# Performance work log

Hardware: AMD Instinct MI355X
Metric: run time of the kernel (lower is better)

Reference implementation:

```python
import jax, jax.numpy as jnp
import numpy as np

B, DIM, HEADS, AGENT = 16, 256, 8, 49
POOL = 7  # int(sqrt(agent_num))


def _pool_matrix(size, out):
    # PyTorch AdaptiveAvgPool2d bin boundaries: start=floor(i*size/out), end=ceil((i+1)*size/out)
    P = np.zeros((out, size), np.float32)
    for i in range(out):
        s = (i * size) // out
        e = -((-(i + 1) * size) // out)
        P[i, s:e] = 1.0 / (e - s)
    return jnp.asarray(P)


def _forward(x, Wq, Wkv, Wproj, bproj, Wdwc, bdwc,
             an_bias, na_bias, ah_bias, aw_bias, ha_bias, wa_bias, H, W):
    b, c, h, w = x.shape
    n = H * W
    head_dim = c // HEADS
    scale = head_dim ** -0.5
    xt = x.reshape(b, c, n).transpose(0, 2, 1)            # [b, n, c]
    q = xt @ Wq.T                                          # [b, n, c]
    kv = xt @ Wkv.T
    k, v = jnp.split(kv, 2, axis=-1)
    # agent tokens: adaptive avg pool of q over the HxW grid -> 7x7
    qimg = q.reshape(b, H, W, c)
    Ph, Pw = _pool_matrix(H, POOL), _pool_matrix(W, POOL)
    agent = jnp.einsum('ph,qw,bhwc->bpqc', Ph, Pw, qimg).reshape(b, AGENT, c)

    def to_heads(t):
        return t.reshape(b, -1, HEADS, head_dim).transpose(0, 2, 1, 3)

    qh, kh, vh, ah = to_heads(q), to_heads(k), to_heads(v), to_heads(agent)

    # stage 1: agent -> kv attention with interpolated position bias
    pb1 = jax.image.resize(an_bias, (HEADS, AGENT, H, W), method='bilinear').reshape(HEADS, AGENT, n)
    pb2 = (ah_bias + aw_bias).reshape(1, HEADS, AGENT, n)
    pos_bias = pb1[None] + pb2                             # [1/b, h, 49, n]
    agent_attn = jax.nn.softmax(jnp.einsum('bhad,bhnd->bhan', ah * scale, kh) + pos_bias, axis=-1)
    agent_v = jnp.einsum('bhan,bhnd->bhad', agent_attn, vh)  # [b, h, 49, d]

    # stage 2: query -> agent attention
    ab1 = jax.image.resize(na_bias, (HEADS, AGENT, H, W), method='bilinear').reshape(HEADS, AGENT, n).transpose(0, 2, 1)
    ab2 = (ha_bias + wa_bias).reshape(1, HEADS, n, AGENT)
    agent_bias = ab1[None] + ab2                           # [1/b, h, n, 49]
    q_attn = jax.nn.softmax(jnp.einsum('bhnd,bhad->bhna', qh * scale, ah) + agent_bias, axis=-1)
    out = jnp.einsum('bhna,bhad->bhnd', q_attn, agent_v).transpose(0, 2, 1, 3).reshape(b, n, c)

    # depthwise conv residual on v
    vimg = vh.transpose(0, 2, 1, 3).reshape(b, H, W, c).transpose(0, 3, 1, 2)  # [b, c, H, W]
    dw = jax.lax.conv_general_dilated(vimg, Wdwc, (1, 1), 'SAME',
                                      feature_group_count=c,
                                      dimension_numbers=('NCHW', 'OIHW', 'NCHW'))
    dw = dw + bdwc[None, :, None, None]
    out = out + dw.transpose(0, 2, 3, 1).reshape(b, n, c)
    out = out @ Wproj.T + bproj
    return out.transpose(0, 2, 1).reshape(b, c, h, w)


def setup_inputs() -> dict:
    key = jax.random.key(0)
    ks = jax.random.split(key, 12)
    s = 0.02
    return {
        'x': jax.random.normal(ks[0], (B, DIM, 64, 64), jnp.float32),
        'Wq': jax.random.normal(ks[1], (DIM, DIM), jnp.float32) * s,
        'Wkv': jax.random.normal(ks[2], (2 * DIM, DIM), jnp.float32) * s,
        'Wproj': jax.random.normal(ks[3], (DIM, DIM), jnp.float32) * s,
        'bproj': jnp.zeros((DIM,), jnp.float32),
        'Wdwc': jax.random.normal(ks[4], (DIM, 1, 3, 3), jnp.float32) * s,
        'bdwc': jnp.zeros((DIM,), jnp.float32),
        'an_bias': jax.random.normal(ks[5], (HEADS, AGENT, 7, 7), jnp.float32) * s,
        'na_bias': jax.random.normal(ks[6], (HEADS, AGENT, 7, 7), jnp.float32) * s,
        'ah_bias': jax.random.normal(ks[7], (1, HEADS, AGENT, 64, 1), jnp.float32) * s,
        'aw_bias': jax.random.normal(ks[8], (1, HEADS, AGENT, 1, 64), jnp.float32) * s,
        'ha_bias': jax.random.normal(ks[9], (1, HEADS, 64, 1, AGENT), jnp.float32) * s,
        'wa_bias': jax.random.normal(ks[10], (1, HEADS, 1, 64, AGENT), jnp.float32) * s,
        'H': 64,
        'W': 64,
    }


def reference(x, Wq, Wkv, Wproj, bproj, Wdwc, bdwc,
              an_bias, na_bias, ah_bias, aw_bias, ha_bias, wa_bias, H, W):
    return _forward(x, Wq, Wkv, Wproj, bproj, Wdwc, bdwc,
                    an_bias, na_bias, ah_bias, aw_bias, ha_bias, wa_bias, H, W)
```

## Files before the change

kernel.cpp:

```cpp
#include <hip/hip_runtime.h>
#include <hip/hip_bf16.h>
#include <stdint.h>

using bf16 = __hip_bfloat16;

#define SCALE 0.17677669529663687f

typedef short short8 __attribute__((ext_vector_type(8)));
typedef float f32x4 __attribute__((ext_vector_type(4)));

__device__ __forceinline__ float bf2f(bf16 v) { return __bfloat162float(v); }

__device__ __forceinline__ unsigned short f2bf(float f) {
    unsigned int u = __float_as_uint(f);
    unsigned int r = u + 0x7fffu + ((u >> 16) & 1u);
    return (unsigned short)(r >> 16);
}

__device__ __forceinline__ void load8bf(const bf16* p, float* f) {
    uint4 u = *reinterpret_cast<const uint4*>(p);
    f[0] = __uint_as_float(u.x << 16); f[1] = __uint_as_float(u.x & 0xffff0000u);
    f[2] = __uint_as_float(u.y << 16); f[3] = __uint_as_float(u.y & 0xffff0000u);
    f[4] = __uint_as_float(u.z << 16); f[5] = __uint_as_float(u.z & 0xffff0000u);
    f[6] = __uint_as_float(u.w << 16); f[7] = __uint_as_float(u.w & 0xffff0000u);
}

__device__ __forceinline__ void gload16(const void* g, void* l) {
    __builtin_amdgcn_global_load_lds(
        (const __attribute__((address_space(1))) void*)g,
        (__attribute__((address_space(3))) void*)l, 16, 0, 0);
}

__global__ __launch_bounds__(256) void convert_w(
    const float* __restrict__ Wq, const float* __restrict__ Wkv,
    const float* __restrict__ Wp,
    bf16* __restrict__ Wqkv_bf, bf16* __restrict__ Wp_bf)
{
    int row = blockIdx.x, tid = threadIdx.x;
    const float* src; bf16* dst;
    if (row < 768) {
        src = (row < 256) ? Wq + (size_t)row * 256 : Wkv + (size_t)(row - 256) * 256;
        dst = Wqkv_bf + (size_t)row * 256;
    } else {
        src = Wp + (size_t)(row - 768) * 256;
        dst = Wp_bf + (size_t)(row - 768) * 256;
    }
    *reinterpret_cast<unsigned short*>(dst + tid) = f2bf(src[tid]);
}

__global__ __launch_bounds__(256) void qkv_mfma(
    const float* __restrict__ x, const bf16* __restrict__ Wqkv,
    bf16* __restrict__ q, bf16* __restrict__ k, bf16* __restrict__ v)
{
    __shared__ __align__(16) short As[128 * 36];
    __shared__ __align__(16) short Bs[128 * 32];
    const int j0 = blockIdx.x * 128;
    const int b  = blockIdx.y >> 5;
    const int m0 = (blockIdx.y & 31) * 128;
    const int tid = threadIdx.x;
    const int w = tid >> 6, lane = tid & 63;
    const int wm = w & 1, wn = w >> 1;
    const int quad = lane >> 4, ln = lane & 15;

    const float* Ax = x + (size_t)(b * 256) * 4096 + m0;
    const short* Bg = (const short*)Wqkv + (size_t)j0 * 256;
    const int ldrow = lane >> 2;
    const int ldcol = (lane & 3) * 8;
    const int c4 = (tid >> 5) * 4;
    const int p4 = (tid & 31) * 4;

    f32x4 acc[4][4] = {};

    for (int k0 = 0; k0 < 256; k0 += 32) {
        __syncthreads();
        #pragma unroll
        for (int p = 0; p < 2; ++p) {
            int row = w * 32 + p * 16;
            gload16(Bg + (size_t)(row + ldrow) * 256 + k0 + ldcol, Bs + row * 32);
        }
        float4 xr[4];
        #pragma unroll
        for (int j = 0; j < 4; ++j)
            xr[j] = *reinterpret_cast<const float4*>(
                Ax + (size_t)(k0 + c4 + j) * 4096 + p4);
        #pragma unroll
        for (int pp = 0; pp < 4; ++pp) {
            unsigned short t4[4];
            t4[0] = f2bf(((const float*)&xr[0])[pp]);
            t4[1] = f2bf(((const float*)&xr[1])[pp]);
            t4[2] = f2bf(((const float*)&xr[2])[pp]);
            t4[3] = f2bf(((const float*)&xr[3])[pp]);
            *reinterpret_cast<uint2*>(&As[(p4 + pp) * 36 + c4]) =
                *reinterpret_cast<const uint2*>(t4);
        }
        __syncthreads();
        short8 af[4], bfr[4];
        #pragma unroll
        for (int mi = 0; mi < 4; ++mi)
            af[mi] = *reinterpret_cast<const short8*>(&As[(wm * 64 + mi * 16 + ln) * 36 + quad * 8]);
        #pragma unroll
        for (int ni = 0; ni < 4; ++ni)
            bfr[ni] = *reinterpret_cast<const short8*>(&Bs[(wn * 64 + ni * 16 + ln) * 32 + quad * 8]);
        #pragma unroll
        for (int mi = 0; mi < 4; ++mi)
            #pragma unroll
            for (int ni = 0; ni < 4; ++ni)
                acc[mi][ni] = __builtin_amdgcn_mfma_f32_16x16x32_bf16(
                    af[mi], bfr[ni], acc[mi][ni], 0, 0, 0);
    }

    bf16* dst; int cb;
    if (j0 < 256)      { dst = q; cb = j0; }
    else if (j0 < 512) { dst = k; cb = j0 - 256; }
    else               { dst = v; cb = j0 - 512; }
    #pragma unroll
    for (int mi = 0; mi < 4; ++mi)
        #pragma unroll
        for (int r = 0; r < 4; ++r) {
            int pos = m0 + wm * 64 + mi * 16 + quad * 4 + r;
            unsigned short* o = reinterpret_cast<unsigned short*>(
                dst + ((size_t)(b * 4096 + pos)) * 256 + cb + wn * 64 + ln);
            #pragma unroll
            for (int ni = 0; ni < 4; ++ni)
                o[ni * 16] = f2bf(acc[mi][ni][r]);
        }
}

__global__ __launch_bounds__(256) void pool_agent(
    const bf16* __restrict__ q, float* __restrict__ agent)
{
    int bid = blockIdx.x;
    int b = bid / 49, a = bid % 49;
    int py = a / 7, px = a % 7;
    int ys = (py * 64) / 7, ye = ((py + 1) * 64 + 6) / 7;
    int xs = (px * 64) / 7, xe = ((px + 1) * 64 + 6) / 7;
    int ch = threadIdx.x;
    float s = 0.f;
    for (int y = ys; y < ye; ++y)
        for (int x = xs; x < xe; ++x)
            s += bf2f(q[((size_t)(b * 4096) + y * 64 + x) * 256 + ch]);
    agent[((size_t)(b * 49) + a) * 256 + ch] = s / (float)((ye - ys) * (xe - xs));
}

__global__ __launch_bounds__(256) void make_pbias(
    const float* __restrict__ an, const float* __restrict__ ahb,
    const float* __restrict__ awb, float* __restrict__ pbias)
{
    int bid = blockIdx.x;
    __shared__ float bb[49], ay[64], ax[64];
    int tid = threadIdx.x;
    if (tid < 49) bb[tid] = an[(size_t)bid * 49 + tid];
    if (tid < 64) {
        ay[tid] = ahb[(size_t)bid * 64 + tid];
        ax[tid] = awb[(size_t)bid * 64 + tid];
    }
    __syncthreads();
    for (int it = 0; it < 16; ++it) {
        int pos = it * 256 + tid;
        int y = pos >> 6, x = pos & 63;
        float fy = (y + 0.5f) * (7.f / 64.f) - 0.5f; fy = fminf(fmaxf(fy, 0.f), 6.f);
        float fx = (x + 0.5f) * (7.f / 64.f) - 0.5f; fx = fminf(fmaxf(fx, 0.f), 6.f);
        int y0 = (int)fy, x0 = (int)fx;
        int y1 = min(y0 + 1, 6), x1 = min(x0 + 1, 6);
        float wy = fy - y0, wx = fx - x0;
        float val = (1.f - wy) * ((1.f - wx) * bb[y0 * 7 + x0] + wx * bb[y0 * 7 + x1])
                  + wy * ((1.f - wx) * bb[y1 * 7 + x0] + wx * bb[y1 * 7 + x1]);
        pbias[(size_t)bid * 4096 + pos] = val + ay[y] + ax[x];
    }
}

__global__ __launch_bounds__(256) void make_abias2(
    const float* __restrict__ na, const float* __restrict__ hab,
    const float* __restrict__ wab, bf16* __restrict__ ab2)
{
    const int h = blockIdx.x, p0 = blockIdx.y * 256;
    const int tid = threadIdx.x;
    __shared__ float bb[49 * 49];
    __shared__ float hy[64 * 49];
    __shared__ float wxs[64 * 49];
    for (int i = tid; i < 49 * 49; i += 256) bb[i] = na[(size_t)h * 2401 + i];
    for (int i = tid; i < 64 * 49; i += 256) {
        hy[i]  = hab[(size_t)h * 3136 + i];
        wxs[i] = wab[(size_t)h * 3136 + i];
    }
    __syncthreads();
    const int pos = p0 + tid;
    const int y = pos >> 6, x = pos & 63;
    float fy = (y + 0.5f) * (7.f / 64.f) - 0.5f; fy = fminf(fmaxf(fy, 0.f), 6.f);
    float fx = (x + 0.5f) * (7.f / 64.f) - 0.5f; fx = fminf(fmaxf(fx, 0.f), 6.f);
    int y0 = (int)fy, x0 = (int)fx;
    int y1 = min(y0 + 1, 6), x1 = min(x0 + 1, 6);
    float wy = fy - y0, wxv = fx - x0;
    float w00 = (1.f - wy) * (1.f - wxv), w01 = (1.f - wy) * wxv;
    float w10 = wy * (1.f - wxv),        w11 = wy * wxv;
    int g00 = y0 * 7 + x0, g01 = y0 * 7 + x1, g10 = y1 * 7 + x0, g11 = y1 * 7 + x1;
    unsigned short outv[64];
    #pragma unroll
    for (int a = 0; a < 64; ++a) {
        float val = 0.f;
        if (a < 49)
            val = w00 * bb[a * 49 + g00] + w01 * bb[a * 49 + g01]
                + w10 * bb[a * 49 + g10] + w11 * bb[a * 49 + g11]
                + hy[y * 49 + a] + wxs[x * 49 + a];
        outv[(a & 15) * 4 + (a >> 4)] = f2bf(val);
    }
    uint4* dst = reinterpret_cast<uint4*>(
        reinterpret_cast<unsigned short*>(ab2) + ((size_t)(h * 4096) + pos) * 64);
    #pragma unroll
    for (int j = 0; j < 8; ++j) dst[j] = reinterpret_cast<const uint4*>(outv)[j];
}

__global__ __launch_bounds__(256) void stage1(
    const float* __restrict__ agent, const bf16* __restrict__ k,
    const bf16* __restrict__ v, const float* __restrict__ pbias,
    float* __restrict__ part_O, float* __restrict__ part_sum)
{
    const int bid = blockIdx.x;
    const int split = bid & 7, h = (bid >> 3) & 7, b = bid >> 6;
    const int tid = threadIdx.x;
    const int w = tid >> 6, lane = tid & 63;
    const int ln = lane & 15, quad = lane >> 4;

    __shared__ __align__(16) short agLds[64 * 32];
    __shared__ __align__(16) short pLds[64 * 140];
    __shared__ __align__(16) short vtLds[32 * 140];

    for (int i = tid; i < 64 * 32; i += 256) {
        int a = i >> 5, d = i & 31;
        float val = (a < 49) ? agent[((size_t)(b * 49) + a) * 256 + h * 32 + d] : 0.f;
        agLds[i] = (short)f2bf(val);
    }
    __syncthreads();

    const short8 agFrag = *reinterpret_cast<const short8*>(&agLds[(w * 16 + ln) * 32 + quad * 8]);
    const int a_row = w * 16 + quad * 4;

    f32x4 oAcc[2] = {};
    float sacc[4] = {0.f, 0.f, 0.f, 0.f};
    const f32x4 zero4 = {0.f, 0.f, 0.f, 0.f};

    for (int sub = 0; sub < 4; ++sub) {
        const int nbase = split * 512 + sub * 128;
        __syncthreads();
        {
            const int n_loc = tid & 127, dh = (tid >> 7) * 16;
            const short* vr = (const short*)v + ((size_t)(b * 4096) + nbase + n_loc) * 256 + h * 32 + dh;
            uint4 u0 = *reinterpret_cast<const uint4*>(vr);
            uint4 u1 = *reinterpret_cast<const uint4*>(vr + 8);
            unsigned int uu[8] = {u0.x, u0.y, u0.z, u0.w, u1.x, u1.y, u1.z, u1.w};
            #pragma unroll
            for (int j = 0; j < 8; ++j) {
                vtLds[(dh + 2 * j) * 140 + n_loc]     = (short)(uu[j] & 0xffffu);
                vtLds[(dh + 2 * j + 1) * 140 + n_loc] = (short)(uu[j] >> 16);
            }
        }
        short8 kf[8];
        #pragma unroll
        for (int t = 0; t < 8; ++t) {
            int n = nbase + t * 16 + ln;
            kf[t] = *reinterpret_cast<const short8*>(
                (const short*)k + ((size_t)(b * 4096) + n) * 256 + h * 32 + quad * 8);
        }
        #pragma unroll
        for (int t = 0; t < 8; ++t) {
            f32x4 s = __builtin_amdgcn_mfma_f32_16x16x32_bf16(agFrag, kf[t], zero4, 0, 0, 0);
            int n = nbase + t * 16 + ln;
            #pragma unroll
            for (int r = 0; r < 4; ++r) {
                int a = a_row + r;
                float e = 0.f;
                if (a < 49) {
                    float sv = s[r] * SCALE + pbias[((size_t)(h * 49) + a) * 4096 + n];
                    e = __expf(sv);
                }
                sacc[r] += e;
                pLds[(a_row + r) * 140 + t * 16 + ln] = (short)f2bf(e);
            }
        }
        __syncthreads();
        #pragma unroll
        for (int ks = 0; ks < 4; ++ks) {
            short8 pf = *reinterpret_cast<const short8*>(&pLds[(w * 16 + ln) * 140 + ks * 32 + quad * 8]);
            #pragma unroll
            for (int dt = 0; dt < 2; ++dt) {
                short8 vf = *reinterpret_cast<const short8*>(&vtLds[(dt * 16 + ln) * 140 + ks * 32 + quad * 8]);
                oAcc[dt] = __builtin_amdgcn_mfma_f32_16x16x32_bf16(pf, vf, oAcc[dt], 0, 0, 0);
            }
        }
    }

    const size_t obase = ((size_t)((b * 8 + h) * 8 + split)) * 1568;
    #pragma unroll
    for (int dt = 0; dt < 2; ++dt)
        #pragma unroll
        for (int r = 0; r < 4; ++r) {
            int a = a_row + r;
            if (a < 49)
                part_O[obase + a * 32 + dt * 16 + ln] = oAcc[dt][r];
        }
    #pragma unroll
    for (int r = 0; r < 4; ++r) {
        float sv = sacc[r];
        #pragma unroll
        for (int m = 1; m < 16; m <<= 1) sv += __shfl_xor(sv, m, 64);
        if (ln == 0) {
            int a = a_row + r;
            if (a < 49)
                part_sum[((b * 8 + h) * 8 + split) * 49 + a] = sv;
        }
    }
}

__global__ __launch_bounds__(256) void stage1_fin(
    const float* __restrict__ part_O, const float* __restrict__ part_sum,
    bf16* __restrict__ avT)
{
    int bh = blockIdx.x;
    __shared__ float inv[49];
    int tid = threadIdx.x;
    if (tid < 49) {
        float s = 0.f;
        #pragma unroll
        for (int sp = 0; sp < 8; ++sp) s += part_sum[(bh * 8 + sp) * 49 + tid];
        inv[tid] = 1.f / s;
    }
    __syncthreads();
    unsigned short* dst = reinterpret_cast<unsigned short*>(avT) + (size_t)bh * 2048;
    for (int i = tid; i < 2048; i += 256) {
        int d = i >> 6, a = i & 63;
        float val = 0.f;
        if (a < 49) {
            float o = 0.f;
            #pragma unroll
            for (int sp = 0; sp < 8; ++sp)
                o += part_O[((size_t)(bh * 8) + sp) * 1568 + a * 32 + d];
            val = o * inv[a];
        }
        dst[i] = f2bf(val);
    }
}

__global__ __launch_bounds__(256) void stage2_mfma(
    const bf16* __restrict__ q, const bf16* __restrict__ v,
    const float* __restrict__ agent, const bf16* __restrict__ avT,
    const bf16* __restrict__ ab2, const float* __restrict__ wdwc,
    const float* __restrict__ bdwc, bf16* __restrict__ mid)
{
    const int bh = blockIdx.x;
    const int b = bh >> 3, h = bh & 7;
    const int base = blockIdx.y * 256;
    const int tid = threadIdx.x;
    const int w = tid >> 6, lane = tid & 63;
    const int quad = lane >> 4, ln = lane & 15;

    __shared__ __align__(16) short agLds[64 * 32];
    __shared__ __align__(16) short pLds[4][16 * 72];
    __shared__ __align__(16) float oLds[2][64 * 36];
    __shared__ float wdLds[32 * 9];
    __shared__ float bdLds[32];

    for (int i = tid; i < 64 * 32; i += 256) {
        int a = i >> 5, d = i & 31;
        float val = (a < 49) ? agent[((size_t)(b * 49) + a) * 256 + h * 32 + d] : 0.f;
        agLds[i] = (short)f2bf(val);
    }
    for (int i = tid; i < 288; i += 256) wdLds[i] = wdwc[(size_t)(h * 32) * 9 + i];
    if (tid < 32) bdLds[tid] = bdwc[h * 32 + tid];
    __syncthreads();

    short8 agF[4];
    #pragma unroll
    for (int t = 0; t < 4; ++t)
        agF[t] = *reinterpret_cast<const short8*>(&agLds[(t * 16 + ln) * 32 + quad * 8]);

    short8 avF[2][2];
    #pragma unroll
    for (int dt = 0; dt < 2; ++dt)
        #pragma unroll
        for (int kc = 0; kc < 2; ++kc)
            avF[dt][kc] = *reinterpret_cast<const short8*>(
                (const short*)avT + ((size_t)bh * 32 + dt * 16 + ln) * 64 + kc * 32 + quad * 8);

    const int prow = tid >> 2, cl = (tid & 3) * 8;
    const f32x4 zero4 = {0.f, 0.f, 0.f, 0.f};

    for (int sub = 0; sub < 4; ++sub) {
        const int p = sub & 1;
        const int pos0w = base + sub * 64 + w * 16;

        const int posd = base + sub * 64 + prow;
        const int yd = posd >> 6, xd = posd & 63;
        uint4 vpre[9];
        #pragma unroll
        for (int dy = -1; dy <= 1; ++dy)
            #pragma unroll
            for (int dx = -1; dx <= 1; ++dx) {
                int idx = (dy + 1) * 3 + (dx + 1);
                int yy = yd + dy, xx = xd + dx;
                int yc = min(max(yy, 0), 63), xc = min(max(xx, 0), 63);
                uint4 t = *reinterpret_cast<const uint4*>(
                    v + ((size_t)(b * 4096) + yc * 64 + xc) * 256 + h * 32 + cl);
                if ((unsigned)yy >= 64u || (unsigned)xx >= 64u) { t.x = 0; t.y = 0; t.z = 0; t.w = 0; }
                vpre[idx] = t;
            }

        uint2 bpre[4];
        #pragma unroll
        for (int r = 0; r < 4; ++r) {
            int posr = pos0w + quad * 4 + r;
            bpre[r] = *reinterpret_cast<const uint2*>(
                reinterpret_cast<const unsigned short*>(ab2) + ((size_t)(h * 4096) + posr) * 64 + ln * 4);
        }

        short8 qf = *reinterpret_cast<const short8*>(
            (const short*)q + ((size_t)(b * 4096) + pos0w + ln) * 256 + h * 32 + quad * 8);
        f32x4 sT[4];
        #pragma unroll
        for (int t = 0; t < 4; ++t)
            sT[t] = __builtin_amdgcn_mfma_f32_16x16x32_bf16(qf, agF[t], zero4, 0, 0, 0);

        float e[4][4];
        float part[4] = {0.f, 0.f, 0.f, 0.f};
        #pragma unroll
        for (int r = 0; r < 4; ++r) {
            float bias[4];
            bias[0] = __uint_as_float(bpre[r].x << 16);
            bias[1] = __uint_as_float(bpre[r].x & 0xffff0000u);
            bias[2] = __uint_as_float(bpre[r].y << 16);
            bias[3] = __uint_as_float(bpre[r].y & 0xffff0000u);
            #pragma unroll
            for (int t = 0; t < 4; ++t) {
                int a = t * 16 + ln;
                float ev = 0.f;
                if (a < 49) ev = __expf(sT[t][r] * SCALE + bias[t]);
                e[t][r] = ev;
                part[r] += ev;
            }
        }
        #pragma unroll
        for (int r = 0; r < 4; ++r) {
            #pragma unroll
            for (int m = 1; m < 16; m <<= 1) part[r] += __shfl_xor(part[r], m, 64);
            part[r] = 1.f / part[r];
        }

        #pragma unroll
        for (int t = 0; t < 4; ++t)
            #pragma unroll
            for (int r = 0; r < 4; ++r)
                pLds[w][(quad * 4 + r) * 72 + t * 16 + ln] = (short)f2bf(e[t][r] * part[r]);

        f32x4 oAcc[2] = {};
        #pragma unroll
        for (int kc = 0; kc < 2; ++kc) {
            short8 pf = *reinterpret_cast<const short8*>(&pLds[w][ln * 72 + kc * 32 + quad * 8]);
            #pragma unroll
            for (int dt = 0; dt < 2; ++dt)
                oAcc[dt] = __builtin_amdgcn_mfma_f32_16x16x32_bf16(pf, avF[dt][kc], oAcc[dt], 0, 0, 0);
        }

        #pragma unroll
        for (int dt = 0; dt < 2; ++dt)
            #pragma unroll
            for (int r = 0; r < 4; ++r)
                oLds[p][(w * 16 + quad * 4 + r) * 36 + dt * 16 + ln] = oAcc[dt][r];
        __syncthreads();

        {
            float acc[8];
            #pragma unroll
            for (int j = 0; j < 8; ++j) acc[j] = oLds[p][prow * 36 + cl + j] + bdLds[cl + j];
            #pragma unroll
            for (int idx = 0; idx < 9; ++idx) {
                unsigned int uu[4] = {vpre[idx].x, vpre[idx].y, vpre[idx].z, vpre[idx].w};
                float f[8];
                f[0] = __uint_as_float(uu[0] << 16); f[1] = __uint_as_float(uu[0] & 0xffff0000u);
                f[2] = __uint_as_float(uu[1] << 16); f[3] = __uint_as_float(uu[1] & 0xffff0000u);
                f[4] = __uint_as_float(uu[2] << 16); f[5] = __uint_as_float(uu[2] & 0xffff0000u);
                f[6] = __uint_as_float(uu[3] << 16); f[7] = __uint_as_float(uu[3] & 0xffff0000u);
                #pragma unroll
                for (int j = 0; j < 8; ++j)
                    acc[j] = fmaf(wdLds[(cl + j) * 9 + idx], f[j], acc[j]);
            }
            unsigned short o16[8];
            #pragma unroll
            for (int j = 0; j < 8; ++j) o16[j] = f2bf(acc[j]);
            *reinterpret_cast<uint4*>(mid + ((size_t)(b * 4096) + posd) * 256 + h * 32 + cl) =
                *reinterpret_cast<const uint4*>(o16);
        }
    }
}

__global__ __launch_bounds__(256) void proj_mfma(
    const bf16* __restrict__ mid, const bf16* __restrict__ Wp,
    const float* __restrict__ bp, float* __restrict__ out)
{
    __shared__ __align__(16) short As[128 * 32];
    __shared__ __align__(16) short Bs[128 * 32];
    const int m0 = blockIdx.x * 128;
    const int b  = blockIdx.y >> 5;
    const int n0 = (blockIdx.y & 31) * 128;
    const int tid = threadIdx.x;
    const int w = tid >> 6, lane = tid & 63;
    const int wm = w & 1, wn = w >> 1;
    const int quad = lane >> 4, ln = lane & 15;

    const short* Ag = (const short*)Wp + (size_t)m0 * 256;
    const short* Bg = (const short*)mid + ((size_t)(b * 4096 + n0)) * 256;
    const int ldrow = lane >> 2;
    const int ldcol = (lane & 3) * 8;

    f32x4 acc[4][4] = {};

    for (int k0 = 0; k0 < 256; k0 += 32) {
        __syncthreads();
        #pragma unroll
        for (int p = 0; p < 2; ++p) {
            int row = w * 32 + p * 16;
            gload16(Ag + (size_t)(row + ldrow) * 256 + k0 + ldcol, As + row * 32);
            gload16(Bg + (size_t)(row + ldrow) * 256 + k0 + ldcol, Bs + row * 32);
        }
        __syncthreads();
        short8 af[4], bfr[4];
        #pragma unroll
        for (int mi = 0; mi < 4; ++mi)
            af[mi] = *reinterpret_cast<const short8*>(&As[(wm * 64 + mi * 16 + ln) * 32 + quad * 8]);
        #pragma unroll
        for (int ni = 0; ni < 4; ++ni)
            bfr[ni] = *reinterpret_cast<const short8*>(&Bs[(wn * 64 + ni * 16 + ln) * 32 + quad * 8]);
        #pragma unroll
        for (int mi = 0; mi < 4; ++mi)
            #pragma unroll
            for (int ni = 0; ni < 4; ++ni)
                acc[mi][ni] = __builtin_amdgcn_mfma_f32_16x16x32_bf16(
                    af[mi], bfr[ni], acc[mi][ni], 0, 0, 0);
    }

    #pragma unroll
    for (int mi = 0; mi < 4; ++mi)
        #pragma unroll
        for (int r = 0; r < 4; ++r) {
            int ch = m0 + wm * 64 + mi * 16 + quad * 4 + r;
            float bias = bp[ch];
            float* o = out + ((size_t)(b * 256 + ch)) * 4096 + n0 + wn * 64 + ln;
            #pragma unroll
            for (int ni = 0; ni < 4; ++ni)
                o[ni * 16] = acc[mi][ni][r] + bias;
        }
}

extern "C" void kernel_launch(void* const* d_in, const int* in_sizes, int n_in,
                              void* d_out, int out_size, void* d_ws, size_t ws_size,
                              hipStream_t stream)
{
    const float* x       = (const float*)d_in[0];
    const float* Wq      = (const float*)d_in[1];
    const float* Wkv     = (const float*)d_in[2];
    const float* Wproj   = (const float*)d_in[3];
    const float* bproj   = (const float*)d_in[4];
    const float* Wdwc    = (const float*)d_in[5];
    const float* bdwc    = (const float*)d_in[6];
    const float* an_bias = (const float*)d_in[7];
    const float* na_bias = (const float*)d_in[8];
    const float* ah_bias = (const float*)d_in[9];
    const float* aw_bias = (const float*)d_in[10];
    const float* ha_bias = (const float*)d_in[11];
    const float* wa_bias = (const float*)d_in[12];

    char* ws = (char*)d_ws;
    bf16*  q      = (bf16*)(ws + 0);
    bf16*  k      = (bf16*)(ws + 33554432);
    bf16*  v      = (bf16*)(ws + 67108864);
    float* part_O   = (float*)(ws + 100663296);
    float* part_sum = (float*)(ws + 100663296 + 6422528);
    bf16*  mid    = (bf16*)(ws + 100663296);
    float* agent  = (float*)(ws + 134217728);
    bf16*  avT    = (bf16*)(ws + 135020544);
    float* pbias  = (float*)(ws + 135823360);
    bf16*  ab2    = (bf16*)(ws + 142245888);
    bf16*  Wqkv_bf = (bf16*)(ws + 148668416);
    bf16*  Wp_bf   = (bf16*)(ws + 149061632);
    float* out    = (float*)d_out;

    convert_w  <<<dim3(1024),      256, 0, stream>>>(Wq, Wkv, Wproj, Wqkv_bf, Wp_bf);
    qkv_mfma   <<<dim3(6, 512),    256, 0, stream>>>(x, Wqkv_bf, q, k, v);
    pool_agent <<<dim3(784),       256, 0, stream>>>(q, agent);
    make_pbias <<<dim3(392),       256, 0, stream>>>(an_bias, ah_bias, aw_bias, pbias);
    make_abias2<<<dim3(8, 16),     256, 0, stream>>>(na_bias, ha_bias, wa_bias, ab2);
    stage1     <<<dim3(1024),      256, 0, stream>>>(agent, k, v, pbias, part_O, part_sum);
    stage1_fin <<<dim3(128),       256, 0, stream>>>(part_O, part_sum, avT);
    stage2_mfma<<<dim3(128, 16),   256, 0, stream>>>(q, v, agent, avT, ab2, Wdwc, bdwc, mid);
    proj_mfma  <<<dim3(2, 512),    256, 0, stream>>>(mid, Wp_bf, bproj, out);
}
```

Before: 376.9 us.

## Double-buffer QKV GEMM shared tiles and remap blocks for XCD-local reuse

The QKV projection GEMM now uses two LDS buffers. Global loads of x and the weights for the next K-slice are issued before the MFMAs on the current slice, and only one barrier runs per iteration. The grid is flattened to 1D and block IDs are remapped so that all six column tiles of an M tile, and neighbouring M tiles, land on the same XCD to improve L2 reuse of x. This doubles LDS use and raises register pressure from the prefetched float4s, which may lower occupancy.

```diff
diff --git a/kernel.cpp b/kernel.cpp
--- a/kernel.cpp
+++ b/kernel.cpp
@@ -52,11 +52,16 @@
     const float* __restrict__ x, const bf16* __restrict__ Wqkv,
     bf16* __restrict__ q, bf16* __restrict__ k, bf16* __restrict__ v)
 {
-    __shared__ __align__(16) short As[128 * 36];
-    __shared__ __align__(16) short Bs[128 * 32];
-    const int j0 = blockIdx.x * 128;
-    const int b  = blockIdx.y >> 5;
-    const int m0 = (blockIdx.y & 31) * 128;
+    __shared__ __align__(16) short As[2][128 * 36];
+    __shared__ __align__(16) short Bs[2][128 * 32];
+    const int bid = blockIdx.x;
+    const int xcd = bid & 7;
+    const int t   = bid >> 3;
+    const int mt  = xcd * 64 + t / 6;
+    const int j   = t % 6;
+    const int b   = mt >> 5;
+    const int m0  = (mt & 31) * 128;
+    const int j0  = j * 128;
     const int tid = threadIdx.x;
     const int w = tid >> 6, lane = tid & 63;
     const int wm = w & 1, wn = w >> 1;
@@ -71,18 +76,17 @@
 
     f32x4 acc[4][4] = {};
 
-    for (int k0 = 0; k0 < 256; k0 += 32) {
-        __syncthreads();
+    {
         #pragma unroll
         for (int p = 0; p < 2; ++p) {
             int row = w * 32 + p * 16;
-            gload16(Bg + (size_t)(row + ldrow) * 256 + k0 + ldcol, Bs + row * 32);
+            gload16(Bg + (size_t)(row + ldrow) * 256 + ldcol, &Bs[0][row * 32]);
         }
         float4 xr[4];
         #pragma unroll
-        for (int j = 0; j < 4; ++j)
-            xr[j] = *reinterpret_cast<const float4*>(
-                Ax + (size_t)(k0 + c4 + j) * 4096 + p4);
+        for (int jj = 0; jj < 4; ++jj)
+            xr[jj] = *reinterpret_cast<const float4*>(
+                Ax + (size_t)(c4 + jj) * 4096 + p4);
         #pragma unroll
         for (int pp = 0; pp < 4; ++pp) {
             unsigned short t4[4];
@@ -90,23 +94,56 @@
             t4[1] = f2bf(((const float*)&xr[1])[pp]);
             t4[2] = f2bf(((const float*)&xr[2])[pp]);
             t4[3] = f2bf(((const float*)&xr[3])[pp]);
-            *reinterpret_cast<uint2*>(&As[(p4 + pp) * 36 + c4]) =
+            *reinterpret_cast<uint2*>(&As[0][(p4 + pp) * 36 + c4]) =
                 *reinterpret_cast<const uint2*>(t4);
         }
-        __syncthreads();
+    }
+    __syncthreads();
+
+    #pragma unroll
+    for (int ks = 0; ks < 8; ++ks) {
+        const int cur = ks & 1, nxt = cur ^ 1;
+        float4 xr[4];
+        if (ks < 7) {
+            const int k1 = (ks + 1) * 32;
+            #pragma unroll
+            for (int p = 0; p < 2; ++p) {
+                int row = w * 32 + p * 16;
+                gload16(Bg + (size_t)(row + ldrow) * 256 + k1 + ldcol, &Bs[nxt][row * 32]);
+            }
+            #pragma unroll
+            for (int jj = 0; jj < 4; ++jj)
+                xr[jj] = *reinterpret_cast<const float4*>(
+                    Ax + (size_t)(k1 + c4 + jj) * 4096 + p4);
+        }
         short8 af[4], bfr[4];
         #pragma unroll
         for (int mi = 0; mi < 4; ++mi)
-            af[mi] = *reinterpret_cast<const short8*>(&As[(wm * 64 + mi * 16 + ln) * 36 + quad * 8]);
+            af[mi] = *reinterpret_cast<const short8*>(
+                &As[cur][(wm * 64 + mi * 16 + ln) * 36 + quad * 8]);
         #pragma unroll
         for (int ni = 0; ni < 4; ++ni)
-            bfr[ni] = *reinterpret_cast<const short8*>(&Bs[(wn * 64 + ni * 16 + ln) * 32 + quad * 8]);
+            bfr[ni] = *reinterpret_cast<const short8*>(
+                &Bs[cur][(wn * 64 + ni * 16 + ln) * 32 + quad * 8]);
         #pragma unroll
         for (int mi = 0; mi < 4; ++mi)
             #pragma unroll
             for (int ni = 0; ni < 4; ++ni)
                 acc[mi][ni] = __builtin_amdgcn_mfma_f32_16x16x32_bf16(
                     af[mi], bfr[ni], acc[mi][ni], 0, 0, 0);
+        if (ks < 7) {
+            #pragma unroll
+            for (int pp = 0; pp < 4; ++pp) {
+                unsigned short t4[4];
+                t4[0] = f2bf(((const float*)&xr[0])[pp]);
+                t4[1] = f2bf(((const float*)&xr[1])[pp]);
+                t4[2] = f2bf(((const float*)&xr[2])[pp]);
+                t4[3] = f2bf(((const float*)&xr[3])[pp]);
+                *reinterpret_cast<uint2*>(&As[nxt][(p4 + pp) * 36 + c4]) =
+                    *reinterpret_cast<const uint2*>(t4);
+            }
+            __syncthreads();
+        }
     }
 
     bf16* dst; int cb;
@@ -583,7 +620,7 @@
     float* out    = (float*)d_out;
 
     convert_w  <<<dim3(1024),      256, 0, stream>>>(Wq, Wkv, Wproj, Wqkv_bf, Wp_bf);
-    qkv_mfma   <<<dim3(6, 512),    256, 0, stream>>>(x, Wqkv_bf, q, k, v);
+    qkv_mfma   <<<dim3(3072),      256, 0, stream>>>(x, Wqkv_bf, q, k, v);
     pool_agent <<<dim3(784),       256, 0, stream>>>(q, agent);
     make_pbias <<<dim3(392),       256, 0, stream>>>(an_bias, ah_bias, aw_bias, pbias);
     make_abias2<<<dim3(8, 16),     256, 0, stream>>>(na_bias, ha_bias, wa_bias, ab2);
```

Result: slower. 391.8 us (+3.9%).
